# Kernel optimization log

Measured on AMD Instinct MI355X. Metric: run time of the kernel, lower is better.

Reference implementation:

```python
import jax, jax.numpy as jnp
import numpy as np

N_QUBITS = 8
NPC = 15  # params per U_SU4 conv block
C64 = jnp.complex64

# CNOT with control = first tensor factor / second tensor factor
CNOT01 = jnp.array([[1, 0, 0, 0], [0, 1, 0, 0], [0, 0, 0, 1], [0, 0, 1, 0]], dtype=C64)
CNOT10 = jnp.array([[1, 0, 0, 0], [0, 0, 0, 1], [0, 0, 1, 0], [0, 1, 0, 0]], dtype=C64)
I2 = jnp.eye(2, dtype=C64)
PX = jnp.array([[0, 1], [1, 0]], dtype=C64)
PY = jnp.array([[0, -1j], [1j, 0]], dtype=C64)
PZ = jnp.array([[1, 0], [0, -1]], dtype=C64)


def _u3(t, p, l):
    ct, st = jnp.cos(t / 2).astype(C64), jnp.sin(t / 2).astype(C64)
    return jnp.stack([
        jnp.stack([ct, -(jnp.exp(1j * l) * st)]),
        jnp.stack([jnp.exp(1j * p) * st, jnp.exp(1j * (p + l)) * ct]),
    ]).astype(C64)


def _ry(t):
    c, s = jnp.cos(t / 2), jnp.sin(t / 2)
    return jnp.stack([jnp.stack([c, -s]), jnp.stack([s, c])]).astype(C64)


def _rz(t):
    z = jnp.zeros((), C64)
    return jnp.stack([jnp.stack([jnp.exp(-1j * t / 2), z]),
                      jnp.stack([z, jnp.exp(1j * t / 2)])]).astype(C64)


def _su4(p):
    # Compose the 15-parameter U_SU4 block into a single 4x4 unitary
    # (first tensor factor = wires[0], second = wires[1]).
    k = jnp.kron
    M = k(_u3(p[0], p[1], p[2]), _u3(p[3], p[4], p[5]))
    M = CNOT01 @ M
    M = k(_ry(p[6]), _rz(p[7])) @ M
    M = CNOT10 @ M
    M = k(_ry(p[8]), I2) @ M
    M = CNOT01 @ M
    M = k(_u3(p[9], p[10], p[11]), _u3(p[12], p[13], p[14])) @ M
    return M


def _apply_2q(state, U, w0, w1):
    # state: [B, 2]*8, axis (w+1) is wire w (wire 0 = most significant, as in
    # PennyLane AmplitudeEmbedding). Apply 4x4 U on wires (w0, w1).
    state = jnp.moveaxis(state, (w0 + 1, w1 + 1), (-2, -1))
    sh = state.shape
    state = state.reshape(sh[:-2] + (4,)) @ U.T
    state = state.reshape(sh)
    return jnp.moveaxis(state, (-2, -1), (w0 + 1, w1 + 1))


def _apply_1q(state, U, w):
    state = jnp.moveaxis(state, w + 1, -1)
    state = state @ U.T
    return jnp.moveaxis(state, -1, w + 1)


def _expval(state, P, w):
    phi = _apply_1q(state, P, w)
    return jnp.sum(jnp.conj(state) * phi, axis=tuple(range(1, N_QUBITS + 1))).real


LAYER1 = [(0, 1), (2, 3), (4, 5), (6, 7), (1, 2), (3, 4), (5, 6), (7, 0)]
LAYER2 = [(2, 4), (6, 0), (0, 2), (4, 6)]
LAYER3 = [(2, 6)]
LAYERS = [LAYER1, LAYER1, LAYER2, LAYER2, LAYER3]


def setup_inputs() -> dict:
    key = jax.random.key(0)
    kx, kw = jax.random.split(key)
    x = jax.random.normal(kx, (32768, 256), dtype=jnp.float32)
    quantum_weights = jax.random.normal(kw, (5 * NPC,), dtype=jnp.float32)
    return {"x": x, "quantum_weights": quantum_weights}


def reference(x, quantum_weights):
    B = x.shape[0]
    # AmplitudeEmbedding with normalize=True
    norm = jnp.linalg.norm(x, axis=1, keepdims=True)
    state = (x / norm).astype(C64).reshape((B,) + (2,) * N_QUBITS)
    for li, pairs in enumerate(LAYERS):
        M = _su4(quantum_weights[li * NPC:(li + 1) * NPC])
        for (a, b) in pairs:
            state = _apply_2q(state, M, a, b)
    # latent_dim == 6: X,Y,Z on wire 2 then wire 6
    outs = [_expval(state, P, wq) for wq in (2, 6) for P in (PX, PY, PZ)]
    return jnp.stack(outs, axis=1)  # [B, 6]
```

## Files before the change

### kernel.cpp

```cpp
#include <hip/hip_runtime.h>

#define DIM 256

__device__ float2 g_M[5 * 16];

__device__ inline float2 cmulc(float2 a, float2 b) {
    return make_float2(a.x * b.x - a.y * b.y, a.x * b.y + a.y * b.x);
}
__device__ inline float2 caddc(float2 a, float2 b) {
    return make_float2(a.x + b.x, a.y + b.y);
}


__device__ void mat_u3(float t, float p, float l, float2* U) {
    float s, c;
    sincosf(0.5f * t, &s, &c);
    float sp, cp, sl, cl, spl, cpl;
    sincosf(p, &sp, &cp);
    sincosf(l, &sl, &cl);
    sincosf(p + l, &spl, &cpl);
    U[0] = make_float2(c, 0.f);
    U[1] = make_float2(-cl * s, -sl * s);
    U[2] = make_float2(cp * s, sp * s);
    U[3] = make_float2(cpl * c, spl * c);
}
__device__ void mat_ry(float t, float2* U) {
    float s, c;
    sincosf(0.5f * t, &s, &c);
    U[0] = make_float2(c, 0.f); U[1] = make_float2(-s, 0.f);
    U[2] = make_float2(s, 0.f); U[3] = make_float2(c, 0.f);
}
__device__ void mat_rz(float t, float2* U) {
    float s, c;
    sincosf(0.5f * t, &s, &c);
    U[0] = make_float2(c, -s); U[1] = make_float2(0.f, 0.f);
    U[2] = make_float2(0.f, 0.f); U[3] = make_float2(c, s);
}
__device__ void mat_I2(float2* U) {
    U[0] = make_float2(1.f, 0.f); U[1] = make_float2(0.f, 0.f);
    U[2] = make_float2(0.f, 0.f); U[3] = make_float2(1.f, 0.f);
}
__device__ void kron4(const float2* A, const float2* B, float2* K) {
    for (int i0 = 0; i0 < 2; ++i0)
        for (int i1 = 0; i1 < 2; ++i1)
            for (int j0 = 0; j0 < 2; ++j0)
                for (int j1 = 0; j1 < 2; ++j1)
                    K[(2 * i0 + i1) * 4 + (2 * j0 + j1)] = cmulc(A[i0 * 2 + j0], B[i1 * 2 + j1]);
}
__device__ void mm4(const float2* A, const float2* B, float2* C) {
    for (int r = 0; r < 4; ++r)
        for (int c = 0; c < 4; ++c) {
            float2 acc = make_float2(0.f, 0.f);
            for (int k = 0; k < 4; ++k) acc = caddc(acc, cmulc(A[r * 4 + k], B[k * 4 + c]));
            C[r * 4 + c] = acc;
        }
}
__device__ void swap_rows(float2* M, int r1, int r2) {
    for (int c = 0; c < 4; ++c) {
        float2 t = M[r1 * 4 + c]; M[r1 * 4 + c] = M[r2 * 4 + c]; M[r2 * 4 + c] = t;
    }
}

__global__ void qsvdd_setup(const float* __restrict__ w) {
    int l = threadIdx.x;
    if (l >= 5) return;
    const float* p = w + l * 15;
    float2 A[4], Bm[4], K[16], M[16], T[16];
    mat_u3(p[0], p[1], p[2], A);
    mat_u3(p[3], p[4], p[5], Bm);
    kron4(A, Bm, M);
    swap_rows(M, 2, 3);
    mat_ry(p[6], A); mat_rz(p[7], Bm);
    kron4(A, Bm, K); mm4(K, M, T);
    swap_rows(T, 1, 3);
    mat_ry(p[8], A); mat_I2(Bm);
    kron4(A, Bm, K); mm4(K, T, M);
    swap_rows(M, 2, 3);
    mat_u3(p[9], p[10], p[11], A);
    mat_u3(p[12], p[13], p[14], Bm);
    kron4(A, Bm, K); mm4(K, M, T);
    for (int i = 0; i < 16; ++i) g_M[l * 16 + i] = T[i];
}


__device__ __forceinline__ float rfl(float x) {
    return __int_as_float(__builtin_amdgcn_readfirstlane(__float_as_int(x)));
}

__device__ __forceinline__ float2 fsel(bool c, float2 a, float2 b) {
    return make_float2(c ? a.x : b.x, c ? a.y : b.y);
}

__device__ __forceinline__ void cmadsv(float2& a, float mx, float my, const float2 v) {
    a.x = fmaf(mx, v.x, a.x);
    a.x = fmaf(-my, v.y, a.x);
    a.y = fmaf(mx, v.y, a.y);
    a.y = fmaf(my, v.x, a.y);
}

template <int IP, int IQ>
__device__ __forceinline__ void gate4(float2* v, const float2* M) {
    constexpr int mp = 1 << IP, mq = 1 << IQ;
    const float2 a0 = v[0], a1 = v[mq], a2 = v[mp], a3 = v[mp | mq];
    float2 n[4];
#pragma unroll
    for (int r = 0; r < 4; ++r) {
        float2 acc = make_float2(0.f, 0.f);
        cmadsv(acc, M[r * 4 + 0].x, M[r * 4 + 0].y, a0);
        cmadsv(acc, M[r * 4 + 1].x, M[r * 4 + 1].y, a1);
        cmadsv(acc, M[r * 4 + 2].x, M[r * 4 + 2].y, a2);
        cmadsv(acc, M[r * 4 + 3].x, M[r * 4 + 3].y, a3);
        n[r] = acc;
    }
    v[0] = n[0]; v[mq] = n[1]; v[mp] = n[2]; v[mp | mq] = n[3];
}

template <int R>
__device__ __forceinline__ void bswap(float2* v, bool pb, int ba) {
    constexpr int m = 1 << R;
#pragma unroll
    for (int j = 0; j < 4; ++j) {
        if (j & m) continue;
        const int j1 = j | m;
        float2 s = fsel(pb, v[j], v[j1]);
        float2 r;
        r.x = __int_as_float(__builtin_amdgcn_ds_bpermute(ba, __float_as_int(s.x)));
        r.y = __int_as_float(__builtin_amdgcn_ds_bpermute(ba, __float_as_int(s.y)));
        v[j] = fsel(pb, r, v[j]);
        v[j1] = fsel(pb, v[j1], r);
    }
}

__global__ __launch_bounds__(256) void qsvdd_main(const float* __restrict__ x,
                                                  float* __restrict__ out) {
    const int lane = threadIdx.x & 63;
    const long e = (long)blockIdx.x * 4 + (threadIdx.x >> 6);

    const int ba0 = ((lane ^ 1) << 2), ba1 = ((lane ^ 2) << 2), ba2 = ((lane ^ 4) << 2);
    const int ba3 = ((lane ^ 8) << 2), ba4 = ((lane ^ 16) << 2), ba5 = ((lane ^ 32) << 2);
    const bool p0 = lane & 1, p1 = lane & 2, p2 = lane & 4;
    const bool p3 = lane & 8, p4 = lane & 16, p5 = lane & 32;

    float4 xv = *reinterpret_cast<const float4*>(x + (e << 8) + (lane << 2));
    float ss = xv.x * xv.x + xv.y * xv.y + xv.z * xv.z + xv.w * xv.w;
#pragma unroll
    for (int off = 32; off; off >>= 1) ss += __shfl_xor(ss, off, 64);
    const float inv = rsqrtf(ss);
    float2 v[4];
    v[0] = make_float2(xv.x * inv, 0.f);
    v[1] = make_float2(xv.y * inv, 0.f);
    v[2] = make_float2(xv.z * inv, 0.f);
    v[3] = make_float2(xv.w * inv, 0.f);

    float2 Mm[16];
#define LOADM(L)                                                              \
    {                                                                         \
        const float* gm = reinterpret_cast<const float*>(g_M) + (L) * 32;     \
        _Pragma("unroll") for (int i = 0; i < 16; ++i) {                      \
            Mm[i].x = rfl(gm[2 * i]);                                         \
            Mm[i].y = rfl(gm[2 * i + 1]);                                     \
        }                                                                     \
    }

    LOADM(0);
    gate4<1, 0>(v, Mm);
    bswap<0>(v, p0, ba0); bswap<1>(v, p1, ba1);
    gate4<1, 0>(v, Mm);
    bswap<0>(v, p2, ba2); bswap<1>(v, p3, ba3);
    gate4<1, 0>(v, Mm);
    bswap<0>(v, p4, ba4); bswap<1>(v, p5, ba5);
    gate4<1, 0>(v, Mm);
    bswap<1>(v, p5, ba5);
    gate4<0, 1>(v, Mm);
    bswap<0>(v, p4, ba4); bswap<1>(v, p3, ba3);
    gate4<0, 1>(v, Mm);
    bswap<0>(v, p2, ba2); bswap<1>(v, p1, ba1);
    gate4<0, 1>(v, Mm);
    bswap<0>(v, p0, ba0); bswap<1>(v, p5, ba5);
    gate4<0, 1>(v, Mm);
    LOADM(1);
    bswap<1>(v, p5, ba5);
    gate4<1, 0>(v, Mm);
    bswap<0>(v, p0, ba0); bswap<1>(v, p1, ba1);
    gate4<1, 0>(v, Mm);
    bswap<0>(v, p2, ba2); bswap<1>(v, p3, ba3);
    gate4<1, 0>(v, Mm);
    bswap<0>(v, p4, ba4); bswap<1>(v, p5, ba5);
    gate4<1, 0>(v, Mm);
    bswap<1>(v, p5, ba5);
    gate4<0, 1>(v, Mm);
    bswap<0>(v, p4, ba4); bswap<1>(v, p3, ba3);
    gate4<0, 1>(v, Mm);
    bswap<0>(v, p2, ba2); bswap<1>(v, p1, ba1);
    gate4<0, 1>(v, Mm);
    bswap<0>(v, p0, ba0); bswap<1>(v, p5, ba5);
    gate4<0, 1>(v, Mm);
    LOADM(2);
    bswap<0>(v, p5, ba5);
    gate4<0, 1>(v, Mm);
    bswap<0>(v, p1, ba1); bswap<1>(v, p3, ba3);
    gate4<1, 0>(v, Mm);
    bswap<0>(v, p3, ba3);
    gate4<0, 1>(v, Mm);
    bswap<0>(v, p3, ba3); bswap<1>(v, p1, ba1);
    gate4<0, 1>(v, Mm);
    LOADM(3);
    bswap<0>(v, p3, ba3);
    gate4<1, 0>(v, Mm);
    bswap<0>(v, p3, ba3); bswap<1>(v, p1, ba1);
    gate4<1, 0>(v, Mm);
    bswap<0>(v, p3, ba3);
    gate4<0, 1>(v, Mm);
    bswap<0>(v, p3, ba3); bswap<1>(v, p1, ba1);
    gate4<0, 1>(v, Mm);
    LOADM(4);
    bswap<0>(v, p1, ba1);
    gate4<0, 1>(v, Mm);

    float acc[6];
    {
        const float2 a = v[0], b = v[1], c = v[2], d = v[3];
        acc[0] = (a.x * b.x + a.y * b.y) + (c.x * d.x + c.y * d.y);
        acc[1] = (a.x * b.y - a.y * b.x) + (c.x * d.y - c.y * d.x);
        acc[2] = (a.x * a.x + a.y * a.y) - (b.x * b.x + b.y * b.y)
               + (c.x * c.x + c.y * c.y) - (d.x * d.x + d.y * d.y);
        acc[3] = (a.x * c.x + a.y * c.y) + (b.x * d.x + b.y * d.y);
        acc[4] = (a.x * c.y - a.y * c.x) + (b.x * d.y - b.y * d.x);
        acc[5] = (a.x * a.x + a.y * a.y) - (c.x * c.x + c.y * c.y)
               + (b.x * b.x + b.y * b.y) - (d.x * d.x + d.y * d.y);
    }
    acc[0] *= 2.f; acc[1] *= 2.f; acc[3] *= 2.f; acc[4] *= 2.f;
#pragma unroll
    for (int k = 0; k < 6; ++k) {
#pragma unroll
        for (int off = 32; off; off >>= 1) acc[k] += __shfl_xor(acc[k], off, 64);
    }
    if (lane == 0) {
        float* o = out + e * 6;
        o[0] = acc[0]; o[1] = acc[1]; o[2] = acc[2];
        o[3] = acc[3]; o[4] = acc[4]; o[5] = acc[5];
    }
}

extern "C" void kernel_launch(void* const* d_in, const int* in_sizes, int n_in,
                              void* d_out, int out_size, void* d_ws, size_t ws_size,
                              hipStream_t stream) {
    const float* x = (const float*)d_in[0];
    const float* w = (const float*)d_in[1];
    float* out = (float*)d_out;
    const int B = in_sizes[0] / DIM;

    hipLaunchKernelGGL(qsvdd_setup, dim3(1), dim3(64), 0, stream, w);
    hipLaunchKernelGGL(qsvdd_main, dim3(B / 4), dim3(256), 0, stream, x, out);
}
```

Baseline: 112.8 us.

## Replace bpermute-based qubit swaps with permlane swaps and xor-mixed lane permutes

Reworks the qubit-to-lane remapping schedule so that most exchanges use v_permlane32_swap / v_permlane16_swap, which swap registers across lane halves without LDS traffic, plus unconditional ds_bpermute with a precomputed xor pattern instead of select+bpermute pairs. Matrix loads drop the readfirstlane scalarization, and the gate's first multiply is peeled off the zero accumulator. The goal is fewer cross-lane LDS operations and selects per gate. In exchange the gate ordering and lane mapping are rewritten entirely, which risks wrong qubit placement, and the matrix values may now live in vector rather than scalar registers.

Measured after the change: 132.1 us. 17.1% more time.

```diff
diff --git a/kernel.cpp b/kernel.cpp
--- a/kernel.cpp
+++ b/kernel.cpp
@@ -83,51 +83,69 @@
 }
 
 
-__device__ __forceinline__ float rfl(float x) {
-    return __int_as_float(__builtin_amdgcn_readfirstlane(__float_as_int(x)));
-}
-
-__device__ __forceinline__ float2 fsel(bool c, float2 a, float2 b) {
-    return make_float2(c ? a.x : b.x, c ? a.y : b.y);
-}
-
-__device__ __forceinline__ void cmadsv(float2& a, float mx, float my, const float2 v) {
+__device__ __forceinline__ void cmadf(float2& a, float mx, float my, float2 v) {
     a.x = fmaf(mx, v.x, a.x);
     a.x = fmaf(-my, v.y, a.x);
     a.y = fmaf(mx, v.y, a.y);
     a.y = fmaf(my, v.x, a.y);
 }
+__device__ __forceinline__ float2 cmulf(float mx, float my, float2 v) {
+    float2 r;
+    r.x = mx * v.x; r.x = fmaf(-my, v.y, r.x);
+    r.y = mx * v.y; r.y = fmaf(my, v.x, r.y);
+    return r;
+}
 
 template <int IP, int IQ>
 __device__ __forceinline__ void gate4(float2* v, const float2* M) {
     constexpr int mp = 1 << IP, mq = 1 << IQ;
     const float2 a0 = v[0], a1 = v[mq], a2 = v[mp], a3 = v[mp | mq];
-    float2 n[4];
-#pragma unroll
-    for (int r = 0; r < 4; ++r) {
-        float2 acc = make_float2(0.f, 0.f);
-        cmadsv(acc, M[r * 4 + 0].x, M[r * 4 + 0].y, a0);
-        cmadsv(acc, M[r * 4 + 1].x, M[r * 4 + 1].y, a1);
-        cmadsv(acc, M[r * 4 + 2].x, M[r * 4 + 2].y, a2);
-        cmadsv(acc, M[r * 4 + 3].x, M[r * 4 + 3].y, a3);
-        n[r] = acc;
-    }
-    v[0] = n[0]; v[mq] = n[1]; v[mp] = n[2]; v[mp | mq] = n[3];
+    float2 n0 = cmulf(M[0].x,  M[0].y,  a0);
+    cmadf(n0, M[1].x,  M[1].y,  a1); cmadf(n0, M[2].x,  M[2].y,  a2); cmadf(n0, M[3].x,  M[3].y,  a3);
+    float2 n1 = cmulf(M[4].x,  M[4].y,  a0);
+    cmadf(n1, M[5].x,  M[5].y,  a1); cmadf(n1, M[6].x,  M[6].y,  a2); cmadf(n1, M[7].x,  M[7].y,  a3);
+    float2 n2 = cmulf(M[8].x,  M[8].y,  a0);
+    cmadf(n2, M[9].x,  M[9].y,  a1); cmadf(n2, M[10].x, M[10].y, a2); cmadf(n2, M[11].x, M[11].y, a3);
+    float2 n3 = cmulf(M[12].x, M[12].y, a0);
+    cmadf(n3, M[13].x, M[13].y, a1); cmadf(n3, M[14].x, M[14].y, a2); cmadf(n3, M[15].x, M[15].y, a3);
+    v[0] = n0; v[mq] = n1; v[mp] = n2; v[mp | mq] = n3;
+}
+
+__device__ __forceinline__ void plsw32(float& a, float& b) {
+    asm("v_permlane32_swap_b32 %0, %1" : "+v"(a), "+v"(b));
+}
+__device__ __forceinline__ void plsw16(float& a, float& b) {
+    asm("v_permlane16_swap_b32 %0, %1" : "+v"(a), "+v"(b));
 }
 
 template <int R>
-__device__ __forceinline__ void bswap(float2* v, bool pb, int ba) {
-    constexpr int m = 1 << R;
+__device__ __forceinline__ void pl32(float2* v) {
+    if constexpr (R == 0) {
+        plsw32(v[0].x, v[1].x); plsw32(v[0].y, v[1].y);
+        plsw32(v[2].x, v[3].x); plsw32(v[2].y, v[3].y);
+    } else {
+        plsw32(v[0].x, v[2].x); plsw32(v[0].y, v[2].y);
+        plsw32(v[1].x, v[3].x); plsw32(v[1].y, v[3].y);
+    }
+}
+template <int R>
+__device__ __forceinline__ void pl16(float2* v) {
+    if constexpr (R == 0) {
+        plsw16(v[0].x, v[1].x); plsw16(v[0].y, v[1].y);
+        plsw16(v[2].x, v[3].x); plsw16(v[2].y, v[3].y);
+    } else {
+        plsw16(v[0].x, v[2].x); plsw16(v[0].y, v[2].y);
+        plsw16(v[1].x, v[3].x); plsw16(v[1].y, v[3].y);
+    }
+}
+
+template <int K>
+__device__ __forceinline__ void lswap(float2* v, const int* bsw) {
+    const int a = bsw[K];
 #pragma unroll
     for (int j = 0; j < 4; ++j) {
-        if (j & m) continue;
-        const int j1 = j | m;
-        float2 s = fsel(pb, v[j], v[j1]);
-        float2 r;
-        r.x = __int_as_float(__builtin_amdgcn_ds_bpermute(ba, __float_as_int(s.x)));
-        r.y = __int_as_float(__builtin_amdgcn_ds_bpermute(ba, __float_as_int(s.y)));
-        v[j] = fsel(pb, r, v[j]);
-        v[j1] = fsel(pb, v[j1], r);
+        v[j].x = __int_as_float(__builtin_amdgcn_ds_bpermute(a, __float_as_int(v[j].x)));
+        v[j].y = __int_as_float(__builtin_amdgcn_ds_bpermute(a, __float_as_int(v[j].y)));
     }
 }
 
@@ -136,10 +154,13 @@
     const int lane = threadIdx.x & 63;
     const long e = (long)blockIdx.x * 4 + (threadIdx.x >> 6);
 
-    const int ba0 = ((lane ^ 1) << 2), ba1 = ((lane ^ 2) << 2), ba2 = ((lane ^ 4) << 2);
-    const int ba3 = ((lane ^ 8) << 2), ba4 = ((lane ^ 16) << 2), ba5 = ((lane ^ 32) << 2);
-    const bool p0 = lane & 1, p1 = lane & 2, p2 = lane & 4;
-    const bool p3 = lane & 8, p4 = lane & 16, p5 = lane & 32;
+    int bsw[4];
+#pragma unroll
+    for (int k = 0; k < 4; ++k) {
+        const int d = ((lane >> k) ^ (lane >> 5)) & 1;
+        const int m = d ? ((1 << k) | 32) : 0;
+        bsw[k] = (lane ^ m) << 2;
+    }
 
     float4 xv = *reinterpret_cast<const float4*>(x + (e << 8) + (lane << 2));
     float ss = xv.x * xv.x + xv.y * xv.y + xv.z * xv.z + xv.w * xv.w;
@@ -153,68 +174,82 @@
     v[3] = make_float2(xv.w * inv, 0.f);
 
     float2 Mm[16];
-#define LOADM(L)                                                              \
-    {                                                                         \
-        const float* gm = reinterpret_cast<const float*>(g_M) + (L) * 32;     \
-        _Pragma("unroll") for (int i = 0; i < 16; ++i) {                      \
-            Mm[i].x = rfl(gm[2 * i]);                                         \
-            Mm[i].y = rfl(gm[2 * i + 1]);                                     \
-        }                                                                     \
+#define LOADM(L)                                                      \
+    {                                                                 \
+        _Pragma("unroll") for (int i = 0; i < 16; ++i)                \
+            Mm[i] = g_M[(L) * 16 + i];                                \
     }
 
     LOADM(0);
     gate4<1, 0>(v, Mm);
-    bswap<0>(v, p0, ba0); bswap<1>(v, p1, ba1);
-    gate4<1, 0>(v, Mm);
-    bswap<0>(v, p2, ba2); bswap<1>(v, p3, ba3);
-    gate4<1, 0>(v, Mm);
-    bswap<0>(v, p4, ba4); bswap<1>(v, p5, ba5);
-    gate4<1, 0>(v, Mm);
-    bswap<1>(v, p5, ba5);
-    gate4<0, 1>(v, Mm);
-    bswap<0>(v, p4, ba4); bswap<1>(v, p3, ba3);
-    gate4<0, 1>(v, Mm);
-    bswap<0>(v, p2, ba2); bswap<1>(v, p1, ba1);
-    gate4<0, 1>(v, Mm);
-    bswap<0>(v, p0, ba0); bswap<1>(v, p5, ba5);
+    lswap<0>(v, bsw); pl32<0>(v);
+    lswap<1>(v, bsw); pl32<1>(v);
+    gate4<1, 0>(v, Mm);
+    lswap<2>(v, bsw); pl32<0>(v);
+    lswap<3>(v, bsw); pl32<1>(v);
+    gate4<1, 0>(v, Mm);
+    lswap<0>(v, bsw); pl32<0>(v);
+    pl16<1>(v);
+    gate4<0, 1>(v, Mm);
+    pl16<0>(v);
+    gate4<1, 0>(v, Mm);
+    pl32<0>(v);
+    lswap<0>(v, bsw); pl32<1>(v);
+    gate4<0, 1>(v, Mm);
+    lswap<3>(v, bsw); pl32<0>(v);
+    lswap<2>(v, bsw); pl32<1>(v);
+    gate4<0, 1>(v, Mm);
+    lswap<1>(v, bsw); pl32<0>(v);
+    pl16<1>(v);
     gate4<0, 1>(v, Mm);
     LOADM(1);
-    bswap<1>(v, p5, ba5);
-    gate4<1, 0>(v, Mm);
-    bswap<0>(v, p0, ba0); bswap<1>(v, p1, ba1);
-    gate4<1, 0>(v, Mm);
-    bswap<0>(v, p2, ba2); bswap<1>(v, p3, ba3);
-    gate4<1, 0>(v, Mm);
-    bswap<0>(v, p4, ba4); bswap<1>(v, p5, ba5);
-    gate4<1, 0>(v, Mm);
-    bswap<1>(v, p5, ba5);
-    gate4<0, 1>(v, Mm);
-    bswap<0>(v, p4, ba4); bswap<1>(v, p3, ba3);
-    gate4<0, 1>(v, Mm);
-    bswap<0>(v, p2, ba2); bswap<1>(v, p1, ba1);
-    gate4<0, 1>(v, Mm);
-    bswap<0>(v, p0, ba0); bswap<1>(v, p5, ba5);
+    pl16<1>(v);
+    gate4<1, 0>(v, Mm);
+    pl32<0>(v);
+    lswap<1>(v, bsw); pl32<1>(v);
+    gate4<1, 0>(v, Mm);
+    lswap<0>(v, bsw); pl32<0>(v);
+    lswap<2>(v, bsw); pl32<1>(v);
+    gate4<0, 1>(v, Mm);
+    pl16<0>(v);
+    lswap<3>(v, bsw); pl32<1>(v);
+    gate4<0, 1>(v, Mm);
+    pl16<0>(v);
+    gate4<1, 0>(v, Mm);
+    pl32<0>(v);
+    lswap<3>(v, bsw); pl32<1>(v);
+    gate4<0, 1>(v, Mm);
+    lswap<2>(v, bsw); pl32<0>(v);
+    lswap<0>(v, bsw); pl32<1>(v);
+    gate4<0, 1>(v, Mm);
+    lswap<1>(v, bsw); pl32<0>(v);
+    pl16<1>(v);
     gate4<0, 1>(v, Mm);
     LOADM(2);
-    bswap<0>(v, p5, ba5);
-    gate4<0, 1>(v, Mm);
-    bswap<0>(v, p1, ba1); bswap<1>(v, p3, ba3);
-    gate4<1, 0>(v, Mm);
-    bswap<0>(v, p3, ba3);
-    gate4<0, 1>(v, Mm);
-    bswap<0>(v, p3, ba3); bswap<1>(v, p1, ba1);
-    gate4<0, 1>(v, Mm);
+    lswap<3>(v, bsw); pl32<0>(v);
+    lswap<1>(v, bsw); pl32<1>(v);
+    gate4<0, 1>(v, Mm);
+    pl32<0>(v);
+    pl16<1>(v);
+    gate4<1, 0>(v, Mm);
+    pl32<1>(v);
+    gate4<0, 1>(v, Mm);
+    pl32<0>(v);
+    pl16<1>(v);
+    gate4<1, 0>(v, Mm);
     LOADM(3);
-    bswap<0>(v, p3, ba3);
-    gate4<1, 0>(v, Mm);
-    bswap<0>(v, p3, ba3); bswap<1>(v, p1, ba1);
-    gate4<1, 0>(v, Mm);
-    bswap<0>(v, p3, ba3);
-    gate4<0, 1>(v, Mm);
-    bswap<0>(v, p3, ba3); bswap<1>(v, p1, ba1);
+    pl16<0>(v);
+    gate4<0, 1>(v, Mm);
+    pl16<0>(v);
+    pl32<1>(v);
+    gate4<0, 1>(v, Mm);
+    pl16<0>(v);
+    gate4<1, 0>(v, Mm);
+    pl32<0>(v);
+    pl16<1>(v);
     gate4<0, 1>(v, Mm);
     LOADM(4);
-    bswap<0>(v, p1, ba1);
+    pl32<0>(v);
     gate4<0, 1>(v, Mm);
 
     float acc[6];
```

## Drop readfirstlane matrix loads, permute both lanes' values, start gate with multiply

Applied to the files above, without the earlier changes.

Each bit swap now permutes both partner amplitudes with ds_bpermute and selects the result afterwards. The old code selected a value, permuted it, then selected again, and the new form removes the select that sat ahead of each permute. This doubles the bpermute count per swap. The readfirstlane wrappers on gate-matrix loads are removed, leaving scalarisation of the uniform loads to the compiler, which may put them in vector registers. Each gate row also starts with a multiply instead of a multiply-add onto zero.

Result: slower. 145.5 us (+28.9%).

```diff
diff --git a/kernel.cpp b/kernel.cpp
--- a/kernel.cpp
+++ b/kernel.cpp
@@ -83,36 +83,39 @@
 }
 
 
-__device__ __forceinline__ float rfl(float x) {
-    return __int_as_float(__builtin_amdgcn_readfirstlane(__float_as_int(x)));
-}
-
-__device__ __forceinline__ float2 fsel(bool c, float2 a, float2 b) {
-    return make_float2(c ? a.x : b.x, c ? a.y : b.y);
-}
-
-__device__ __forceinline__ void cmadsv(float2& a, float mx, float my, const float2 v) {
+__device__ __forceinline__ void cmadf(float2& a, float mx, float my, float2 v) {
     a.x = fmaf(mx, v.x, a.x);
     a.x = fmaf(-my, v.y, a.x);
     a.y = fmaf(mx, v.y, a.y);
     a.y = fmaf(my, v.x, a.y);
 }
+__device__ __forceinline__ float2 cmulf(float mx, float my, float2 v) {
+    float2 r;
+    r.x = mx * v.x; r.x = fmaf(-my, v.y, r.x);
+    r.y = mx * v.y; r.y = fmaf(my, v.x, r.y);
+    return r;
+}
 
 template <int IP, int IQ>
 __device__ __forceinline__ void gate4(float2* v, const float2* M) {
     constexpr int mp = 1 << IP, mq = 1 << IQ;
     const float2 a0 = v[0], a1 = v[mq], a2 = v[mp], a3 = v[mp | mq];
-    float2 n[4];
-#pragma unroll
-    for (int r = 0; r < 4; ++r) {
-        float2 acc = make_float2(0.f, 0.f);
-        cmadsv(acc, M[r * 4 + 0].x, M[r * 4 + 0].y, a0);
-        cmadsv(acc, M[r * 4 + 1].x, M[r * 4 + 1].y, a1);
-        cmadsv(acc, M[r * 4 + 2].x, M[r * 4 + 2].y, a2);
-        cmadsv(acc, M[r * 4 + 3].x, M[r * 4 + 3].y, a3);
-        n[r] = acc;
-    }
-    v[0] = n[0]; v[mq] = n[1]; v[mp] = n[2]; v[mp | mq] = n[3];
+    float2 n0 = cmulf(M[0].x,  M[0].y,  a0);
+    cmadf(n0, M[1].x,  M[1].y,  a1); cmadf(n0, M[2].x,  M[2].y,  a2); cmadf(n0, M[3].x,  M[3].y,  a3);
+    float2 n1 = cmulf(M[4].x,  M[4].y,  a0);
+    cmadf(n1, M[5].x,  M[5].y,  a1); cmadf(n1, M[6].x,  M[6].y,  a2); cmadf(n1, M[7].x,  M[7].y,  a3);
+    float2 n2 = cmulf(M[8].x,  M[8].y,  a0);
+    cmadf(n2, M[9].x,  M[9].y,  a1); cmadf(n2, M[10].x, M[10].y, a2); cmadf(n2, M[11].x, M[11].y, a3);
+    float2 n3 = cmulf(M[12].x, M[12].y, a0);
+    cmadf(n3, M[13].x, M[13].y, a1); cmadf(n3, M[14].x, M[14].y, a2); cmadf(n3, M[15].x, M[15].y, a3);
+    v[0] = n0; v[mq] = n1; v[mp] = n2; v[mp | mq] = n3;
+}
+
+__device__ __forceinline__ float2 bperm2(int ba, float2 s) {
+    float2 r;
+    r.x = __int_as_float(__builtin_amdgcn_ds_bpermute(ba, __float_as_int(s.x)));
+    r.y = __int_as_float(__builtin_amdgcn_ds_bpermute(ba, __float_as_int(s.y)));
+    return r;
 }
 
 template <int R>
@@ -122,12 +125,12 @@
     for (int j = 0; j < 4; ++j) {
         if (j & m) continue;
         const int j1 = j | m;
-        float2 s = fsel(pb, v[j], v[j1]);
-        float2 r;
-        r.x = __int_as_float(__builtin_amdgcn_ds_bpermute(ba, __float_as_int(s.x)));
-        r.y = __int_as_float(__builtin_amdgcn_ds_bpermute(ba, __float_as_int(s.y)));
-        v[j] = fsel(pb, r, v[j]);
-        v[j1] = fsel(pb, v[j1], r);
+        const float2 r0 = bperm2(ba, v[j]);
+        const float2 r1 = bperm2(ba, v[j1]);
+        v[j].x  = pb ? r1.x : v[j].x;
+        v[j].y  = pb ? r1.y : v[j].y;
+        v[j1].x = pb ? v[j1].x : r0.x;
+        v[j1].y = pb ? v[j1].y : r0.y;
     }
 }
 
@@ -153,13 +156,10 @@
     v[3] = make_float2(xv.w * inv, 0.f);
 
     float2 Mm[16];
-#define LOADM(L)                                                              \
-    {                                                                         \
-        const float* gm = reinterpret_cast<const float*>(g_M) + (L) * 32;     \
-        _Pragma("unroll") for (int i = 0; i < 16; ++i) {                      \
-            Mm[i].x = rfl(gm[2 * i]);                                         \
-            Mm[i].y = rfl(gm[2 * i + 1]);                                     \
-        }                                                                     \
+#define LOADM(L)                                                      \
+    {                                                                 \
+        _Pragma("unroll") for (int i = 0; i < 16; ++i)                \
+            Mm[i] = g_M[(L) * 16 + i];                                \
     }
 
     LOADM(0);
```
